# Optimization experiments

Measured on AMD Instinct MI355X. Metric: run time of the kernel, lower is better.

The kernel has to match this reference:

```python
import jax, jax.numpy as jnp
import numpy as np
from jax import lax

E, H, O, T = 1024, 2048, 2, 2048

def setup_inputs() -> dict:
    key = jax.random.key(0)
    ks = jax.random.split(key, 10)
    sc = lambda k, shape: (jax.random.normal(k, shape, dtype=jnp.float32) * 0.02)
    return {
        "h0": jax.random.normal(ks[0], (1, 1, H), dtype=jnp.float32),
        "c0": jax.random.normal(ks[1], (1, 1, H), dtype=jnp.float32),
        "ground_truth": jax.random.normal(ks[2], (1, T, O), dtype=jnp.float32),
        "use_gt": jax.random.randint(ks[3], (T,), 0, 2, dtype=jnp.int32),
        "W_emb": sc(ks[4], (E, O)), "b_emb": jnp.zeros((E,), jnp.float32),
        "W_ih": sc(ks[5], (4 * H, E)), "b_ih": jnp.zeros((4 * H,), jnp.float32),
        "W_hh": sc(ks[6], (4 * H, H)), "b_hh": jnp.zeros((4 * H,), jnp.float32),
        "W_out": sc(ks[7], (O, H)), "b_out": jnp.zeros((O,), jnp.float32),
        "output_length": T,
    }

def reference(h0, c0, ground_truth, use_gt, W_emb, b_emb, W_ih, b_ih, W_hh, b_hh, W_out, b_out, output_length):
    h = h0.reshape(-1)            # [H]
    c = c0.reshape(-1)            # [H]
    gt = ground_truth[0]          # [T, 2]
    # initial input: embedding of ones([1,2])
    x0 = W_emb @ jnp.ones((O,), jnp.float32) + b_emb  # [E]

    def step(carry, inp):
        h, c, x = carry
        gt_t, ug = inp
        gates = W_ih @ x + b_ih + W_hh @ h + b_hh      # [4H], PyTorch gate order i,f,g,o
        i, f, g, o = jnp.split(gates, 4)
        c_new = jax.nn.sigmoid(f) * c + jax.nn.sigmoid(i) * jnp.tanh(g)
        h_new = jax.nn.sigmoid(o) * jnp.tanh(c_new)
        raw = W_out @ h_new + b_out                    # [2]
        loss_t = jnp.mean((raw - gt_t) ** 2)           # MSELoss per step
        nxt = jnp.where(ug == 1, gt_t, raw)            # teacher forcing branch
        x_new = W_emb @ nxt + b_emb
        return (h_new, c_new, x_new), (raw, loss_t)

    (_, _, _), (preds, losses) = lax.scan(
        step, (h, c, x0), (gt[:output_length], use_gt[:output_length]))
    return preds, jnp.sum(losses)
```

## Files before the change

kernel.cpp:

```cpp
#include <hip/hip_runtime.h>

#define NWG   256
#define NTHR  256
#define TT    2048
#define HH    2048
#define EE    1024

__device__ __forceinline__ float wred(float v){
  v += __shfl_xor(v, 1, 64);
  v += __shfl_xor(v, 2, 64);
  v += __shfl_xor(v, 4, 64);
  v += __shfl_xor(v, 8, 64);
  v += __shfl_xor(v, 16, 64);
  v += __shfl_xor(v, 32, 64);
  return v;
}

__device__ __forceinline__ float sigm(float x){ return 1.0f / (1.0f + __expf(-x)); }

extern "C" __global__ void __launch_bounds__(NTHR, 1)
lstm_seq_kernel(const float* __restrict__ h0, const float* __restrict__ c0,
                const float* __restrict__ gt, const int* __restrict__ ugt,
                const float* __restrict__ W_emb, const float* __restrict__ b_emb,
                const float* __restrict__ W_ih, const float* __restrict__ b_ih,
                const float* __restrict__ W_hh, const float* __restrict__ b_hh,
                const float* __restrict__ W_out, const float* __restrict__ b_out,
                float* __restrict__ out, unsigned long long* __restrict__ hbuf)
{
  const int wgid = blockIdx.x;
  const int tid  = threadIdx.x;
  const int gw   = tid >> 6;
  const int l    = tid & 63;
  const int j0   = wgid * 8;

  __shared__ float h_lds[HH];
  __shared__ float gates_lds[4][8];

  float2 whh[8][16];
  #pragma unroll
  for (int u = 0; u < 8; ++u){
    const float* rp = W_hh + (size_t)(2048*gw + j0 + u) * HH;
    #pragma unroll
    for (int i = 0; i < 16; ++i)
      whh[u][i] = *(const float2*)(rp + 2*l + 128*i);
  }
  float2 wo0[16], wo1[16];
  #pragma unroll
  for (int i = 0; i < 16; ++i){
    wo0[i] = *(const float2*)(W_out + 2*l + 128*i);
    wo1[i] = *(const float2*)(W_out + HH + 2*l + 128*i);
  }
  const float bo0 = b_out[0], bo1 = b_out[1];

  float aE0[8], aE1[8], aB[8];
  #pragma unroll
  for (int u = 0; u < 8; ++u){ aE0[u] = 0.f; aE1[u] = 0.f; aB[u] = 0.f; }
  for (int i = 0; i < 16; ++i){
    const int k = l + 64*i;
    const float2 we = *(const float2*)(W_emb + 2*k);
    const float be = b_emb[k];
    #pragma unroll
    for (int u = 0; u < 8; ++u){
      const float wv = W_ih[(size_t)(2048*gw + j0 + u)*EE + k];
      aE0[u] = fmaf(wv, we.x, aE0[u]);
      aE1[u] = fmaf(wv, we.y, aE1[u]);
      aB[u]  = fmaf(wv, be,  aB[u]);
    }
  }
  float myE0 = 0.f, myE1 = 0.f, myB = 0.f;
  #pragma unroll
  for (int u = 0; u < 8; ++u){
    const float e0 = wred(aE0[u]);
    const float e1 = wred(aE1[u]);
    const float bb = wred(aB[u]);
    if (l == u){
      const int r = 2048*gw + j0 + u;
      myE0 = e0; myE1 = e1; myB = bb + b_ih[r] + b_hh[r];
    }
  }

  float c_state = (gw == 0 && l < 8) ? c0[j0 + l] : 0.f;

  for (int t = 0; t < TT; ++t){
    float g0 = 0.f, g1 = 0.f; int ug = 0;
    if (t > 0){
      g0 = gt[2*(t-1)]; g1 = gt[2*(t-1)+1]; ug = ugt[t-1];
    }

    const int e0i = (gw << 9) + l;
    if (t == 0){
      #pragma unroll
      for (int i = 0; i < 8; ++i)
        h_lds[e0i + (i<<6)] = h0[e0i + (i<<6)];
    } else {
      const unsigned long long* bp = hbuf + ((t-1)&1)*HH + e0i;
      const unsigned tagexp = (unsigned)t;
      unsigned fresh = 0; int rounds = 0;
      while (fresh != 0xFFu){
        unsigned long long v[8];
        #pragma unroll
        for (int i = 0; i < 8; ++i)
          v[i] = __hip_atomic_load(bp + (i<<6), __ATOMIC_RELAXED, __HIP_MEMORY_SCOPE_AGENT);
        #pragma unroll
        for (int i = 0; i < 8; ++i){
          if (!(fresh & (1u<<i)) && (unsigned)(v[i] >> 32) == tagexp){
            h_lds[e0i + (i<<6)] = __uint_as_float((unsigned)v[i]);
            fresh |= (1u<<i);
          }
        }
        if (++rounds > 16384) break;
      }
    }
    __syncthreads();

    float ga[8];
    #pragma unroll
    for (int u = 0; u < 8; ++u) ga[u] = 0.f;
    float r0 = 0.f, r1 = 0.f;
    #pragma unroll
    for (int i = 0; i < 16; ++i){
      const float2 hv = *(const float2*)(h_lds + 2*l + 128*i);
      r0 = fmaf(wo0[i].x, hv.x, r0); r0 = fmaf(wo0[i].y, hv.y, r0);
      r1 = fmaf(wo1[i].x, hv.x, r1); r1 = fmaf(wo1[i].y, hv.y, r1);
      #pragma unroll
      for (int u = 0; u < 8; ++u){
        ga[u] = fmaf(whh[u][i].x, hv.x, ga[u]);
        ga[u] = fmaf(whh[u][i].y, hv.y, ga[u]);
      }
    }
    #pragma unroll
    for (int u = 0; u < 8; ++u) ga[u] = wred(ga[u]);
    r0 = wred(r0); r1 = wred(r1);

    const float raw0 = r0 + bo0, raw1 = r1 + bo1;
    float n0, n1;
    if (t == 0){ n0 = 1.f; n1 = 1.f; }
    else {
      if (wgid == 0 && tid == 0){
        out[2*(t-1)]   = raw0;
        out[2*(t-1)+1] = raw1;
      }
      n0 = (ug == 1) ? g0 : raw0;
      n1 = (ug == 1) ? g1 : raw1;
    }

    if (l < 8){
      float gate = ga[0];
      #pragma unroll
      for (int u = 1; u < 8; ++u) if (l == u) gate = ga[u];
      gate += fmaf(myE0, n0, fmaf(myE1, n1, myB));
      gates_lds[gw][l] = gate;
    }
    __syncthreads();

    if (gw == 0 && l < 8){
      const float gi = gates_lds[0][l], gf = gates_lds[1][l];
      const float gg = gates_lds[2][l], go = gates_lds[3][l];
      const float cn = sigm(gf)*c_state + sigm(gi)*tanhf(gg);
      const float hn = sigm(go)*tanhf(cn);
      c_state = cn;
      const unsigned long long pk =
          ((unsigned long long)(unsigned)(t + 1) << 32) |
          (unsigned long long)__float_as_uint(hn);
      __hip_atomic_store(hbuf + (t&1)*HH + j0 + l, pk, __ATOMIC_RELAXED, __HIP_MEMORY_SCOPE_AGENT);
    }
  }

  if (wgid != 0) return;

  {
    const int e0i = (gw << 9) + l;
    const unsigned long long* bp = hbuf + ((TT-1)&1)*HH + e0i;
    const unsigned tagexp = (unsigned)TT;
    unsigned fresh = 0; int rounds = 0;
    while (fresh != 0xFFu){
      unsigned long long v[8];
      #pragma unroll
      for (int i = 0; i < 8; ++i)
        v[i] = __hip_atomic_load(bp + (i<<6), __ATOMIC_RELAXED, __HIP_MEMORY_SCOPE_AGENT);
      #pragma unroll
      for (int i = 0; i < 8; ++i){
        if (!(fresh & (1u<<i)) && (unsigned)(v[i] >> 32) == tagexp){
          h_lds[e0i + (i<<6)] = __uint_as_float((unsigned)v[i]);
          fresh |= (1u<<i);
        }
      }
      if (++rounds > 16384) break;
    }
  }
  __syncthreads();
  if (gw == 0){
    float r0 = 0.f, r1 = 0.f;
    #pragma unroll
    for (int i = 0; i < 16; ++i){
      const float2 hv = *(const float2*)(h_lds + 2*l + 128*i);
      r0 = fmaf(wo0[i].x, hv.x, r0); r0 = fmaf(wo0[i].y, hv.y, r0);
      r1 = fmaf(wo1[i].x, hv.x, r1); r1 = fmaf(wo1[i].y, hv.y, r1);
    }
    r0 = wred(r0); r1 = wred(r1);
    if (l == 0){
      out[2*(TT-1)]   = r0 + bo0;
      out[2*(TT-1)+1] = r1 + bo1;
    }
  }
}

extern "C" __global__ void loss_kernel(const float* __restrict__ preds,
                                       const float* __restrict__ gt,
                                       float* __restrict__ loss_out)
{
  const int tid = threadIdx.x;
  float acc = 0.f;
  #pragma unroll
  for (int s = 0; s < 8; ++s){
    const int t = tid + 256*s;
    const float d0 = preds[2*t]   - gt[2*t];
    const float d1 = preds[2*t+1] - gt[2*t+1];
    acc += 0.5f*(d0*d0 + d1*d1);
  }
  acc = wred(acc);
  __shared__ float ws[4];
  if ((tid & 63) == 0) ws[tid >> 6] = acc;
  __syncthreads();
  if (tid == 0) loss_out[0] = ws[0] + ws[1] + ws[2] + ws[3];
}

extern "C" void kernel_launch(void* const* d_in, const int* in_sizes, int n_in,
                              void* d_out, int out_size, void* d_ws, size_t ws_size,
                              hipStream_t stream)
{
  (void)in_sizes; (void)n_in; (void)out_size; (void)ws_size;
  const float* h0    = (const float*)d_in[0];
  const float* c0    = (const float*)d_in[1];
  const float* gt    = (const float*)d_in[2];
  const int*   ugt   = (const int*)  d_in[3];
  const float* W_emb = (const float*)d_in[4];
  const float* b_emb = (const float*)d_in[5];
  const float* W_ih  = (const float*)d_in[6];
  const float* b_ih  = (const float*)d_in[7];
  const float* W_hh  = (const float*)d_in[8];
  const float* b_hh  = (const float*)d_in[9];
  const float* W_out = (const float*)d_in[10];
  const float* b_out = (const float*)d_in[11];
  float* out  = (float*)d_out;
  unsigned long long* hbuf = (unsigned long long*)d_ws;

  void* args[] = { &h0, &c0, &gt, &ugt, &W_emb, &b_emb, &W_ih, &b_ih,
                   &W_hh, &b_hh, &W_out, &b_out, &out, &hbuf };
  hipLaunchCooperativeKernel((const void*)lstm_seq_kernel,
                             dim3(NWG), dim3(NTHR), args, 0, stream);

  loss_kernel<<<dim3(1), dim3(NTHR), 0, stream>>>(out, gt, out + 2*TT);
}
```

Before: 9.556 ms.

## Assign all four gates of two hidden units per wave to drop second barrier

Reassigns W_hh/W_ih rows so each wave holds the i,f,g,o rows for two hidden units instead of one gate type for eight units. Every wave can then compute its own cell update in registers, which removes the gates LDS exchange and the second __syncthreads per timestep. The h LDS buffer is double-buffered by timestep parity so the next step's fill does not race with reads from the previous step. The cost is redundant activation maths in all 64 lanes of every wave.

```diff
diff --git a/kernel.cpp b/kernel.cpp
--- a/kernel.cpp
+++ b/kernel.cpp
@@ -32,14 +32,14 @@
   const int gw   = tid >> 6;
   const int l    = tid & 63;
   const int j0   = wgid * 8;
-
-  __shared__ float h_lds[HH];
-  __shared__ float gates_lds[4][8];
+  const int uA   = j0 + 2*gw;
+
+  __shared__ float h_lds[2][HH];
 
   float2 whh[8][16];
   #pragma unroll
   for (int u = 0; u < 8; ++u){
-    const float* rp = W_hh + (size_t)(2048*gw + j0 + u) * HH;
+    const float* rp = W_hh + (size_t)(2048*(u>>1) + uA + (u&1)) * HH;
     #pragma unroll
     for (int i = 0; i < 16; ++i)
       whh[u][i] = *(const float2*)(rp + 2*l + 128*i);
@@ -61,25 +61,22 @@
     const float be = b_emb[k];
     #pragma unroll
     for (int u = 0; u < 8; ++u){
-      const float wv = W_ih[(size_t)(2048*gw + j0 + u)*EE + k];
+      const float wv = W_ih[(size_t)(2048*(u>>1) + uA + (u&1))*EE + k];
       aE0[u] = fmaf(wv, we.x, aE0[u]);
       aE1[u] = fmaf(wv, we.y, aE1[u]);
       aB[u]  = fmaf(wv, be,  aB[u]);
     }
   }
-  float myE0 = 0.f, myE1 = 0.f, myB = 0.f;
+  float e0v[8], e1v[8], bv[8];
   #pragma unroll
   for (int u = 0; u < 8; ++u){
-    const float e0 = wred(aE0[u]);
-    const float e1 = wred(aE1[u]);
-    const float bb = wred(aB[u]);
-    if (l == u){
-      const int r = 2048*gw + j0 + u;
-      myE0 = e0; myE1 = e1; myB = bb + b_ih[r] + b_hh[r];
-    }
-  }
-
-  float c_state = (gw == 0 && l < 8) ? c0[j0 + l] : 0.f;
+    const int r = 2048*(u>>1) + uA + (u&1);
+    e0v[u] = wred(aE0[u]);
+    e1v[u] = wred(aE1[u]);
+    bv[u]  = wred(aB[u]) + b_ih[r] + b_hh[r];
+  }
+
+  float cA = c0[uA], cB = c0[uA + 1];
 
   for (int t = 0; t < TT; ++t){
     float g0 = 0.f, g1 = 0.f; int ug = 0;
@@ -87,11 +84,12 @@
       g0 = gt[2*(t-1)]; g1 = gt[2*(t-1)+1]; ug = ugt[t-1];
     }
 
+    float* hl = h_lds[t & 1];
     const int e0i = (gw << 9) + l;
     if (t == 0){
       #pragma unroll
       for (int i = 0; i < 8; ++i)
-        h_lds[e0i + (i<<6)] = h0[e0i + (i<<6)];
+        hl[e0i + (i<<6)] = h0[e0i + (i<<6)];
     } else {
       const unsigned long long* bp = hbuf + ((t-1)&1)*HH + e0i;
       const unsigned tagexp = (unsigned)t;
@@ -104,7 +102,7 @@
         #pragma unroll
         for (int i = 0; i < 8; ++i){
           if (!(fresh & (1u<<i)) && (unsigned)(v[i] >> 32) == tagexp){
-            h_lds[e0i + (i<<6)] = __uint_as_float((unsigned)v[i]);
+            hl[e0i + (i<<6)] = __uint_as_float((unsigned)v[i]);
             fresh |= (1u<<i);
           }
         }
@@ -119,7 +117,7 @@
     float r0 = 0.f, r1 = 0.f;
     #pragma unroll
     for (int i = 0; i < 16; ++i){
-      const float2 hv = *(const float2*)(h_lds + 2*l + 128*i);
+      const float2 hv = *(const float2*)(hl + 2*l + 128*i);
       r0 = fmaf(wo0[i].x, hv.x, r0); r0 = fmaf(wo0[i].y, hv.y, r0);
       r1 = fmaf(wo1[i].x, hv.x, r1); r1 = fmaf(wo1[i].y, hv.y, r1);
       #pragma unroll
@@ -144,31 +142,28 @@
       n1 = (ug == 1) ? g1 : raw1;
     }
 
-    if (l < 8){
-      float gate = ga[0];
-      #pragma unroll
-      for (int u = 1; u < 8; ++u) if (l == u) gate = ga[u];
-      gate += fmaf(myE0, n0, fmaf(myE1, n1, myB));
-      gates_lds[gw][l] = gate;
-    }
-    __syncthreads();
-
-    if (gw == 0 && l < 8){
-      const float gi = gates_lds[0][l], gf = gates_lds[1][l];
-      const float gg = gates_lds[2][l], go = gates_lds[3][l];
-      const float cn = sigm(gf)*c_state + sigm(gi)*tanhf(gg);
-      const float hn = sigm(go)*tanhf(cn);
-      c_state = cn;
+    float gf[8];
+    #pragma unroll
+    for (int u = 0; u < 8; ++u)
+      gf[u] = ga[u] + fmaf(e0v[u], n0, fmaf(e1v[u], n1, bv[u]));
+    const float cAn = sigm(gf[2])*cA + sigm(gf[0])*tanhf(gf[4]);
+    const float hA  = sigm(gf[6])*tanhf(cAn); cA = cAn;
+    const float cBn = sigm(gf[3])*cB + sigm(gf[1])*tanhf(gf[5]);
+    const float hB  = sigm(gf[7])*tanhf(cBn); cB = cBn;
+
+    if (l < 2){
+      const float hv = (l == 0) ? hA : hB;
       const unsigned long long pk =
           ((unsigned long long)(unsigned)(t + 1) << 32) |
-          (unsigned long long)__float_as_uint(hn);
-      __hip_atomic_store(hbuf + (t&1)*HH + j0 + l, pk, __ATOMIC_RELAXED, __HIP_MEMORY_SCOPE_AGENT);
+          (unsigned long long)__float_as_uint(hv);
+      __hip_atomic_store(hbuf + (t&1)*HH + uA + l, pk, __ATOMIC_RELAXED, __HIP_MEMORY_SCOPE_AGENT);
     }
   }
 
   if (wgid != 0) return;
 
   {
+    float* hl = h_lds[0];
     const int e0i = (gw << 9) + l;
     const unsigned long long* bp = hbuf + ((TT-1)&1)*HH + e0i;
     const unsigned tagexp = (unsigned)TT;
@@ -181,7 +176,7 @@
       #pragma unroll
       for (int i = 0; i < 8; ++i){
         if (!(fresh & (1u<<i)) && (unsigned)(v[i] >> 32) == tagexp){
-          h_lds[e0i + (i<<6)] = __uint_as_float((unsigned)v[i]);
+          hl[e0i + (i<<6)] = __uint_as_float((unsigned)v[i]);
           fresh |= (1u<<i);
         }
       }
@@ -190,10 +185,11 @@
   }
   __syncthreads();
   if (gw == 0){
+    const float* hl = h_lds[0];
     float r0 = 0.f, r1 = 0.f;
     #pragma unroll
     for (int i = 0; i < 16; ++i){
-      const float2 hv = *(const float2*)(h_lds + 2*l + 128*i);
+      const float2 hv = *(const float2*)(hl + 2*l + 128*i);
       r0 = fmaf(wo0[i].x, hv.x, r0); r0 = fmaf(wo0[i].y, hv.y, r0);
       r1 = fmaf(wo1[i].x, hv.x, r1); r1 = fmaf(wo1[i].y, hv.y, r1);
     }
```

Measured after the change: 9.110 ms. -4.7%, faster.
